# Optimization experiments

Measured on AMD Instinct MI355X. Metric: run time of the kernel, lower is better.

## Reference

```python
import jax, jax.numpy as jnp
import numpy as np

N, E = 20000, 320000
NFEAT, NHID = 512, 1024
DROPOUT_P = 0.5


def setup_inputs() -> dict:
    key = jax.random.key(0)
    ks = jax.random.split(key, 9)
    x = jax.random.normal(ks[0], (N, NFEAT), dtype=jnp.float32)
    W1 = jax.random.normal(ks[1], (NFEAT, NHID), dtype=jnp.float32) / np.sqrt(NFEAT)
    b1 = jnp.zeros((NHID,), dtype=jnp.float32)
    W2 = jax.random.normal(ks[2], (NHID, NFEAT), dtype=jnp.float32) / np.sqrt(NHID)
    b2 = jnp.zeros((NFEAT,), dtype=jnp.float32)
    adj_vals = jax.random.uniform(ks[3], (E,), dtype=jnp.float32)
    u_drop = jax.random.uniform(ks[4], (N, NHID), dtype=jnp.float32)
    src = jax.random.randint(ks[5], (E,), 0, N, dtype=jnp.int64)
    dst = jax.random.randint(ks[6], (E,), 0, N, dtype=jnp.int64)
    return {"x": x, "W1": W1, "b1": b1, "W2": W2, "b2": b2,
            "adj_vals": adj_vals, "u_drop": u_drop, "src": src, "dst": dst}


def _graph_conv(h, W, b, adj_vals, src, dst, n_nodes):
    # GraphConvolution: adj @ (h @ W) + b, with adj in COO form (src, dst, vals)
    support = h @ W                                   # [N, d_out]
    msgs = adj_vals[:, None] * support[src]           # [E, d_out]
    agg = jax.ops.segment_sum(msgs, dst, num_segments=n_nodes)
    return agg + b


def reference(x, W1, b1, W2, b2, adj_vals, u_drop, src, dst):
    h = jax.nn.relu(_graph_conv(x, W1, b1, adj_vals, src, dst, N))
    # inverted dropout (training=True), deterministic via u_drop
    keep = (u_drop > DROPOUT_P).astype(h.dtype) / (1.0 - DROPOUT_P)
    h = h * keep
    out = _graph_conv(h, W2, b2, adj_vals, src, dst, N)
    return out
```

## Files before the change

kernel.cpp:

```cpp
#include <hip/hip_runtime.h>
#include <hip/hip_bf16.h>

typedef __attribute__((ext_vector_type(8))) short short8;
typedef __attribute__((ext_vector_type(4))) float f32x4;

#define N_NODES 20000
#define N_EDGES 320000
#define NFEAT 512
#define NHID 1024
#define MBTOT 1252
#define SCAN_NB 79

__device__ __forceinline__ float bf2f(unsigned short u) {
    union { unsigned int i; float f; } c; c.i = ((unsigned int)u) << 16; return c.f;
}
__device__ __forceinline__ unsigned short f2bf(float f) {
    union { float f; unsigned int i; } c; c.f = f;
    unsigned int x = c.i;
    return (unsigned short)((x + 0x7fffu + ((x >> 16) & 1u)) >> 16);
}


__global__ void hist_kernel(const int* __restrict__ dst, int* __restrict__ deg, int E) {
    int e = blockIdx.x * 256 + threadIdx.x;
    if (e < E) atomicAdd(&deg[dst[e]], 1);
}

__global__ __launch_bounds__(256) void scan_a(const int* __restrict__ deg,
                                              int* __restrict__ rp,
                                              int* __restrict__ part, int n) {
    __shared__ int sd[256];
    int t = threadIdx.x;
    int i = blockIdx.x * 256 + t;
    int v = (i < n) ? deg[i] : 0;
    int acc = v;
    sd[t] = acc;
    __syncthreads();
    for (int off = 1; off < 256; off <<= 1) {
        int u = (t >= off) ? sd[t - off] : 0;
        __syncthreads();
        acc += u;
        sd[t] = acc;
        __syncthreads();
    }
    if (i < n) rp[i] = acc - v;
    if (t == 255) part[blockIdx.x] = acc;
}

__global__ __launch_bounds__(256) void scan_b(int* __restrict__ part, int nb) {
    __shared__ int sd[256];
    int t = threadIdx.x;
    int v = (t < nb) ? part[t] : 0;
    int acc = v;
    sd[t] = acc;
    __syncthreads();
    for (int off = 1; off < 256; off <<= 1) {
        int u = (t >= off) ? sd[t - off] : 0;
        __syncthreads();
        acc += u;
        sd[t] = acc;
        __syncthreads();
    }
    if (t < nb) part[t] = acc - v;
    if (t == 255) part[nb] = acc;
}

__global__ __launch_bounds__(256) void scan_c(int* __restrict__ rp, int* __restrict__ cursor,
                                              const int* __restrict__ part, int n, int nb) {
    int i = blockIdx.x * 256 + threadIdx.x;
    if (i < n) {
        int v = rp[i] + part[blockIdx.x];
        rp[i] = v;
        cursor[i] = v;
    }
    if (i == 0) rp[n] = part[nb];
}

__global__ void fill_kernel(const int* __restrict__ src, const int* __restrict__ dst,
                            const float* __restrict__ vals, int* __restrict__ cursor,
                            int2* __restrict__ csr_ov, int E) {
    int e = blockIdx.x * 256 + threadIdx.x;
    if (e < E) {
        int d = dst[e];
        int pos = atomicAdd(&cursor[d], 1);
        csr_ov[pos] = make_int2(src[e] << 10, __float_as_int(vals[e]));
    }
}


__device__ __forceinline__ void transpose_body(const float* __restrict__ W,
                                               unsigned short* __restrict__ Bp,
                                               int K, int N, int bid) {
    __shared__ float tile[32][33];
    const int KT = K >> 5;
    int ntx = N >> 5;
    int k0 = (bid / ntx) << 5;
    int n0 = (bid % ntx) << 5;
    int tx = threadIdx.x & 31, ty = threadIdx.x >> 5;
#pragma unroll
    for (int i = 0; i < 32; i += 8)
        tile[ty + i][tx] = W[(size_t)(k0 + ty + i) * N + n0 + tx];
    __syncthreads();
#pragma unroll
    for (int i = 0; i < 32; i += 8) {
        int n = n0 + ty + i;
        int k = k0 + tx;
        int nb = n >> 4, rl = n & 15;
        int kb = k >> 5, kq = (k & 31) >> 3, j = k & 7;
        Bp[((((size_t)nb * KT + kb) * 64) + kq * 16 + rl) * 8 + j] = f2bf(tile[tx][ty + i]);
    }
}

__global__ __launch_bounds__(256) void transpose2_kernel(const float* __restrict__ W1,
                                                         unsigned short* __restrict__ w1p,
                                                         const float* __restrict__ W2,
                                                         unsigned short* __restrict__ w2p) {
    if (blockIdx.x < 512) transpose_body(W1, w1p, NFEAT, NHID, blockIdx.x);
    else                  transpose_body(W2, w2p, NHID, NFEAT, blockIdx.x - 512);
}


__global__ __launch_bounds__(256) void prep_kernel(const float* __restrict__ x,
                                                   unsigned short* __restrict__ xb,
                                                   const float* __restrict__ u,
                                                   unsigned int* __restrict__ mask) {
    __shared__ unsigned char nib[256];
    int b = blockIdx.x;
    int t = threadIdx.x;
    if (b < 5000) {
        int i = b * 256 + t;
        f32x4 v0 = ((const f32x4*)x)[i * 2];
        f32x4 v1 = ((const f32x4*)x)[i * 2 + 1];
        short8 o;
#pragma unroll
        for (int j = 0; j < 4; ++j) {
            o[j]     = (short)f2bf(v0[j]);
            o[4 + j] = (short)f2bf(v1[j]);
        }
        ((short8*)xb)[i] = o;
    } else {
        size_t base = (size_t)(b - 5000) * 2048;
        f32x4 v0 = ((const f32x4*)(u + base))[t * 2];
        f32x4 v1 = ((const f32x4*)(u + base))[t * 2 + 1];
        unsigned n = 0;
#pragma unroll
        for (int j = 0; j < 4; ++j) {
            n |= (v0[j] > 0.5f ? 1u : 0u) << j;
            n |= (v1[j] > 0.5f ? 1u : 0u) << (4 + j);
        }
        nib[t] = (unsigned char)n;
        __syncthreads();
        if (t < 64) {
            unsigned w = (unsigned)nib[t * 4] | ((unsigned)nib[t * 4 + 1] << 8) |
                         ((unsigned)nib[t * 4 + 2] << 16) | ((unsigned)nib[t * 4 + 3] << 24);
            mask[base / 32 + t] = w;
        }
    }
}


__global__ __launch_bounds__(256) void agg1_kernel(const unsigned short* __restrict__ xbf,
                                                   const int2* __restrict__ csr_ov,
                                                   const int* __restrict__ row_ptr,
                                                   unsigned short* __restrict__ A1p) {
    const int c = blockIdx.x & 7;
    const int dbase = (blockIdx.x >> 3) * 32;
    const int wid = threadIdx.x >> 6;
    const int lane = threadIdx.x & 63;
    const int g = lane >> 3;
    const int s = lane & 7;
    const int d = dbase + wid * 8 + g;
    const int e0 = row_ptr[d], e1 = row_ptr[d + 1];
    const char* xc = (const char*)xbf + (c * 64 + s * 8) * 2;
    const int glane = g * 8;

    f32x4 a0 = {0.f, 0.f, 0.f, 0.f}, a1 = {0.f, 0.f, 0.f, 0.f};

    int offX = 0; float valX = 0.f;
    if (e0 + s < e1) { int2 t = csr_ov[e0 + s]; offX = t.x; valX = __int_as_float(t.y); }

    for (int eb = e0; eb < e1; eb += 8) {
        int offY = 0; float valY = 0.f;
        if (eb + 8 + s < e1) { int2 t = csr_ov[eb + 8 + s]; offY = t.x; valY = __int_as_float(t.y); }
        int cnt = e1 - eb; if (cnt > 8) cnt = 8;
        if (cnt == 8) {
            short8 w[8];
#pragma unroll
            for (int i = 0; i < 8; ++i)
                w[i] = *(const short8*)(xc + __shfl(offX, glane + i));
#pragma unroll
            for (int i = 0; i < 8; ++i) {
                float val = __shfl(valX, glane + i);
#pragma unroll
                for (int j = 0; j < 4; ++j) {
                    a0[j] += val * bf2f((unsigned short)w[i][j]);
                    a1[j] += val * bf2f((unsigned short)w[i][4 + j]);
                }
            }
        } else {
            for (int i = 0; i < cnt; ++i) {
                int off = __shfl(offX, glane + i);
                float val = __shfl(valX, glane + i);
                short8 w = *(const short8*)(xc + off);
#pragma unroll
                for (int j = 0; j < 4; ++j) {
                    a0[j] += val * bf2f((unsigned short)w[j]);
                    a1[j] += val * bf2f((unsigned short)w[4 + j]);
                }
            }
        }
        offX = offY; valX = valY;
    }
    short8 o;
#pragma unroll
    for (int j = 0; j < 4; ++j) {
        o[j]     = (short)f2bf(a0[j]);
        o[4 + j] = (short)f2bf(a1[j]);
    }
    size_t idx = ((((size_t)(d >> 4) * (NFEAT / 32) + (c * 2 + (s >> 2))) * 64) +
                  (s & 3) * 16 + (d & 15)) * 8;
    *(short8*)&A1p[idx] = o;
}


__global__ __launch_bounds__(256) void agg2_kernel(const unsigned short* __restrict__ s2,
                                                   const int2* __restrict__ csr_ov,
                                                   const int* __restrict__ row_ptr,
                                                   const float* __restrict__ b2,
                                                   float* __restrict__ out) {
    const int c = blockIdx.x & 7;
    const int dbase = (blockIdx.x >> 3) * 32;
    const int wid = threadIdx.x >> 6;
    const int lane = threadIdx.x & 63;
    const int g = lane >> 3;
    const int s = lane & 7;
    const int d = dbase + wid * 8 + g;
    const int e0 = row_ptr[d], e1 = row_ptr[d + 1];
    const int fb = c * 64 + s * 8;
    const char* xc = (const char*)s2 + fb * 2;
    const int glane = g * 8;

    f32x4 a0 = *(const f32x4*)&b2[fb];
    f32x4 a1 = *(const f32x4*)&b2[fb + 4];

    int offX = 0; float valX = 0.f;
    if (e0 + s < e1) { int2 t = csr_ov[e0 + s]; offX = t.x; valX = __int_as_float(t.y); }

    for (int eb = e0; eb < e1; eb += 8) {
        int offY = 0; float valY = 0.f;
        if (eb + 8 + s < e1) { int2 t = csr_ov[eb + 8 + s]; offY = t.x; valY = __int_as_float(t.y); }
        int cnt = e1 - eb; if (cnt > 8) cnt = 8;
        if (cnt == 8) {
            short8 w[8];
#pragma unroll
            for (int i = 0; i < 8; ++i)
                w[i] = *(const short8*)(xc + __shfl(offX, glane + i));
#pragma unroll
            for (int i = 0; i < 8; ++i) {
                float val = __shfl(valX, glane + i);
#pragma unroll
                for (int j = 0; j < 4; ++j) {
                    a0[j] += val * bf2f((unsigned short)w[i][j]);
                    a1[j] += val * bf2f((unsigned short)w[i][4 + j]);
                }
            }
        } else {
            for (int i = 0; i < cnt; ++i) {
                int off = __shfl(offX, glane + i);
                float val = __shfl(valX, glane + i);
                short8 w = *(const short8*)(xc + off);
#pragma unroll
                for (int j = 0; j < 4; ++j) {
                    a0[j] += val * bf2f((unsigned short)w[j]);
                    a1[j] += val * bf2f((unsigned short)w[4 + j]);
                }
            }
        }
        offX = offY; valX = valY;
    }
    *(f32x4*)&out[(size_t)d * NFEAT + fb]     = a0;
    *(f32x4*)&out[(size_t)d * NFEAT + fb + 4] = a1;
}


template <int EPI, int KT, int NW>
__global__ __launch_bounds__(256, 4) void gemm_pk(
    const unsigned short* __restrict__ Ap,
    const unsigned short* __restrict__ Bp,
    unsigned short* __restrict__ C,
    int M,
    const float* __restrict__ bias,
    const unsigned int* __restrict__ umask) {
    constexpr int N = NW * 64;
    constexpr int MI_MAX = 625;

    const int nwg = gridDim.x;
    const int bid = blockIdx.x;
    const int q = nwg >> 3, r = nwg & 7;
    const int xcd = bid & 7, pos = bid >> 3;
    const int swz = (xcd < r ? xcd * (q + 1) : r * (q + 1) + (xcd - r) * q) + pos;

    const int wid = threadIdx.x >> 6;
    const int lane = threadIdx.x & 63;
    const int rl = lane & 15;
    const int kq = lane >> 4;

    constexpr int NT2 = NW / 2;
    const int bm = swz / NT2;
    const int bn = swz % NT2;
    int mi = bm * 2 + (wid >> 1); if (mi >= MI_MAX) mi = MI_MAX - 1;
    const int ni = bn * 2 + (wid & 1);

    const unsigned short* ab = Ap + (size_t)(mi * 2) * KT * 512 + lane * 8;
    const unsigned short* bb = Bp + (size_t)(ni * 4) * KT * 512 + lane * 8;

    f32x4 acc[2][4] = {};
    short8 aX[2], bX[4], aY[2], bY[4];

#pragma unroll
    for (int m = 0; m < 2; ++m) aX[m] = *(const short8*)(ab + (size_t)m * KT * 512);
#pragma unroll
    for (int n = 0; n < 4; ++n) bX[n] = *(const short8*)(bb + (size_t)n * KT * 512);

#pragma unroll 1
    for (int kb = 0; kb < KT; kb += 2) {
#pragma unroll
        for (int m = 0; m < 2; ++m)
            aY[m] = *(const short8*)(ab + ((size_t)m * KT + kb + 1) * 512);
#pragma unroll
        for (int n = 0; n < 4; ++n)
            bY[n] = *(const short8*)(bb + ((size_t)n * KT + kb + 1) * 512);
#pragma unroll
        for (int m = 0; m < 2; ++m)
#pragma unroll
            for (int n = 0; n < 4; ++n)
                acc[m][n] = __builtin_amdgcn_mfma_f32_16x16x32_bf16(aX[m], bX[n], acc[m][n], 0, 0, 0);
        if (kb + 2 < KT) {
#pragma unroll
            for (int m = 0; m < 2; ++m)
                aX[m] = *(const short8*)(ab + ((size_t)m * KT + kb + 2) * 512);
#pragma unroll
            for (int n = 0; n < 4; ++n)
                bX[n] = *(const short8*)(bb + ((size_t)n * KT + kb + 2) * 512);
        }
#pragma unroll
        for (int m = 0; m < 2; ++m)
#pragma unroll
            for (int n = 0; n < 4; ++n)
                acc[m][n] = __builtin_amdgcn_mfma_f32_16x16x32_bf16(aY[m], bY[n], acc[m][n], 0, 0, 0);
    }

    if constexpr (EPI == 1) {
        __shared__ unsigned short ltr[4][32][40];
        constexpr int KT2 = N / 32;
#pragma unroll
        for (int n2 = 0; n2 < 2; ++n2) {
#pragma unroll
            for (int m = 0; m < 2; ++m) {
#pragma unroll
                for (int nn = 0; nn < 2; ++nn) {
                    int n = n2 * 2 + nn;
                    float bv = bias[ni * 64 + n * 16 + rl];
#pragma unroll
                    for (int j = 0; j < 4; ++j) {
                        float v = acc[m][n][j] + bv;
                        v = v > 0.f ? v : 0.f;
                        ltr[wid][m * 16 + kq * 4 + j][nn * 16 + rl] = f2bf(v);
                    }
                }
            }
            __builtin_amdgcn_s_waitcnt(0);
#pragma unroll
            for (int m2 = 0; m2 < 2; ++m2) {
                int row = m2 * 16 + rl;
                int gr = mi * 32 + row;
                unsigned w = umask[(size_t)gr * (N >> 5) + (ni * 2 + n2)];
                short8 u = *(const short8*)&ltr[wid][row][kq * 8];
                short8 o;
#pragma unroll
                for (int j = 0; j < 4; ++j) {
                    o[j]     = ((w >> (kq * 8 + j)) & 1u)
                               ? (short)f2bf(bf2f((unsigned short)u[j]) * 2.0f) : (short)0;
                    o[4 + j] = ((w >> (kq * 8 + 4 + j)) & 1u)
                               ? (short)f2bf(bf2f((unsigned short)u[4 + j]) * 2.0f) : (short)0;
                }
                int mbg = mi * 2 + m2;
                size_t dst = (((size_t)mbg * KT2 + (ni * 2 + n2)) * 64 + lane) * 8;
                *(short8*)&C[dst] = o;
            }
            __builtin_amdgcn_s_waitcnt(0);
        }
    } else {
        const int crow = kq * 4;
#pragma unroll
        for (int m = 0; m < 2; ++m) {
#pragma unroll
            for (int n = 0; n < 4; ++n) {
                int gr0 = mi * 32 + m * 16 + crow;
                int gc = ni * 64 + n * 16 + rl;
#pragma unroll
                for (int j = 0; j < 4; ++j) {
                    int gr = gr0 + j;
                    if (gr < M)
                        C[(size_t)gr * N + gc] = f2bf(acc[m][n][j]);
                }
            }
        }
    }
}


extern "C" void kernel_launch(void* const* d_in, const int* in_sizes, int n_in,
                              void* d_out, int out_size, void* d_ws, size_t ws_size,
                              hipStream_t stream) {
    const float* x        = (const float*)d_in[0];
    const float* W1       = (const float*)d_in[1];
    const float* b1       = (const float*)d_in[2];
    const float* W2       = (const float*)d_in[3];
    const float* b2       = (const float*)d_in[4];
    const float* adj_vals = (const float*)d_in[5];
    const float* u_drop   = (const float*)d_in[6];
    const int*   src      = (const int*)d_in[7];
    const int*   dst      = (const int*)d_in[8];
    float* out = (float*)d_out;

    char* p = (char*)d_ws;
    auto take = [&](size_t bytes) {
        char* q = p;
        p += (bytes + 255) & ~(size_t)255;
        return q;
    };
    int* deg        = (int*)take((size_t)N_NODES * 4);
    int* row_ptr    = (int*)take((size_t)(N_NODES + 1) * 4);
    int* cursor     = (int*)take((size_t)N_NODES * 4);
    int* part       = (int*)take((size_t)(SCAN_NB + 1) * 4);
    int2* csr_ov    = (int2*)take((size_t)N_EDGES * 8);
    unsigned short* w1p   = (unsigned short*)take((size_t)NFEAT * NHID * 2);
    unsigned short* w2p   = (unsigned short*)take((size_t)NFEAT * NHID * 2);
    unsigned short* xbf   = (unsigned short*)take((size_t)N_NODES * NFEAT * 2);
    unsigned short* a1p   = (unsigned short*)take((size_t)MBTOT * (NFEAT / 32) * 1024);
    unsigned short* a2p   = (unsigned short*)take((size_t)MBTOT * (NHID / 32) * 1024);
    unsigned short* s2buf = (unsigned short*)take((size_t)N_NODES * NFEAT * 2);
    unsigned int* umask   = (unsigned int*)take((size_t)N_NODES * (NHID / 32) * 4);

    hipMemsetAsync(deg, 0, (size_t)N_NODES * 4, stream);
    hist_kernel<<<(N_EDGES + 255) / 256, 256, 0, stream>>>(dst, deg, N_EDGES);
    scan_a<<<SCAN_NB, 256, 0, stream>>>(deg, row_ptr, part, N_NODES);
    scan_b<<<1, 256, 0, stream>>>(part, SCAN_NB);
    scan_c<<<SCAN_NB, 256, 0, stream>>>(row_ptr, cursor, part, N_NODES, SCAN_NB);
    fill_kernel<<<(N_EDGES + 255) / 256, 256, 0, stream>>>(src, dst, adj_vals, cursor,
                                                           csr_ov, N_EDGES);
    transpose2_kernel<<<1024, 256, 0, stream>>>(W1, w1p, W2, w2p);
    prep_kernel<<<15000, 256, 0, stream>>>(x, xbf, u_drop, umask);

    agg1_kernel<<<8 * 625, 256, 0, stream>>>(xbf, csr_ov, row_ptr, a1p);

    gemm_pk<1, NFEAT / 32, NHID / 64><<<313 * (NHID / 128), 256, 0, stream>>>(
        a1p, w1p, a2p, N_NODES, b1, umask);
    gemm_pk<0, NHID / 32, NFEAT / 64><<<313 * (NFEAT / 128), 256, 0, stream>>>(
        a2p, w2p, s2buf, N_NODES, nullptr, nullptr);

    agg2_kernel<<<8 * 625, 256, 0, stream>>>(s2buf, csr_ov, row_ptr, b2, out);
}
```

Measured before the change: 232.0 us.

## Merge prep, transpose and histogram launches; fuse mask build into agg1; drop shuffle prefetch

Combines the bf16 conversion of x, the two weight transposes and the degree histogram into one launch, and runs the dropout mask construction in the same launch as the first aggregation. This cuts the number of kernel launches and lets independent work fill the GPU together. Both aggregation kernels also drop the per-lane edge prefetch and shuffle broadcast, so every lane now loads the eight CSR entries directly. Those loads are redundant across lanes but served from cache, and the software prefetch of the next batch is lost.

New measurement: 244.8 us. 5.5% more time.

```diff
diff --git a/kernel.cpp b/kernel.cpp
--- a/kernel.cpp
+++ b/kernel.cpp
@@ -20,11 +20,6 @@
     return (unsigned short)((x + 0x7fffu + ((x >> 16) & 1u)) >> 16);
 }
 
-
-__global__ void hist_kernel(const int* __restrict__ dst, int* __restrict__ deg, int E) {
-    int e = blockIdx.x * 256 + threadIdx.x;
-    if (e < E) atomicAdd(&deg[dst[e]], 1);
-}
 
 __global__ __launch_bounds__(256) void scan_a(const int* __restrict__ deg,
                                               int* __restrict__ rp,
@@ -111,20 +106,14 @@
     }
 }
 
-__global__ __launch_bounds__(256) void transpose2_kernel(const float* __restrict__ W1,
-                                                         unsigned short* __restrict__ w1p,
-                                                         const float* __restrict__ W2,
-                                                         unsigned short* __restrict__ w2p) {
-    if (blockIdx.x < 512) transpose_body(W1, w1p, NFEAT, NHID, blockIdx.x);
-    else                  transpose_body(W2, w2p, NHID, NFEAT, blockIdx.x - 512);
-}
-
-
-__global__ __launch_bounds__(256) void prep_kernel(const float* __restrict__ x,
-                                                   unsigned short* __restrict__ xb,
-                                                   const float* __restrict__ u,
-                                                   unsigned int* __restrict__ mask) {
-    __shared__ unsigned char nib[256];
+__global__ __launch_bounds__(256) void p1_kernel(const float* __restrict__ x,
+                                                 unsigned short* __restrict__ xb,
+                                                 const float* __restrict__ W1,
+                                                 unsigned short* __restrict__ w1p,
+                                                 const float* __restrict__ W2,
+                                                 unsigned short* __restrict__ w2p,
+                                                 const int* __restrict__ dst,
+                                                 int* __restrict__ deg) {
     int b = blockIdx.x;
     int t = threadIdx.x;
     if (b < 5000) {
@@ -138,59 +127,69 @@
             o[4 + j] = (short)f2bf(v1[j]);
         }
         ((short8*)xb)[i] = o;
+    } else if (b < 5512) {
+        transpose_body(W1, w1p, NFEAT, NHID, b - 5000);
+    } else if (b < 6024) {
+        transpose_body(W2, w2p, NHID, NFEAT, b - 5512);
     } else {
+        int e = (b - 6024) * 256 + t;
+        if (e < N_EDGES) atomicAdd(&deg[dst[e]], 1);
+    }
+}
+
+
+__global__ __launch_bounds__(256) void p3_kernel(const unsigned short* __restrict__ xbf,
+                                                 const int2* __restrict__ csr_ov,
+                                                 const int* __restrict__ row_ptr,
+                                                 unsigned short* __restrict__ A1p,
+                                                 const float* __restrict__ u,
+                                                 unsigned int* __restrict__ mask) {
+    __shared__ unsigned char nib[256];
+    int b = blockIdx.x;
+    int tt = threadIdx.x;
+    if (b >= 5000) {
         size_t base = (size_t)(b - 5000) * 2048;
-        f32x4 v0 = ((const f32x4*)(u + base))[t * 2];
-        f32x4 v1 = ((const f32x4*)(u + base))[t * 2 + 1];
+        f32x4 v0 = ((const f32x4*)(u + base))[tt * 2];
+        f32x4 v1 = ((const f32x4*)(u + base))[tt * 2 + 1];
         unsigned n = 0;
 #pragma unroll
         for (int j = 0; j < 4; ++j) {
             n |= (v0[j] > 0.5f ? 1u : 0u) << j;
             n |= (v1[j] > 0.5f ? 1u : 0u) << (4 + j);
         }
-        nib[t] = (unsigned char)n;
+        nib[tt] = (unsigned char)n;
         __syncthreads();
-        if (t < 64) {
-            unsigned w = (unsigned)nib[t * 4] | ((unsigned)nib[t * 4 + 1] << 8) |
-                         ((unsigned)nib[t * 4 + 2] << 16) | ((unsigned)nib[t * 4 + 3] << 24);
-            mask[base / 32 + t] = w;
-        }
-    }
-}
-
-
-__global__ __launch_bounds__(256) void agg1_kernel(const unsigned short* __restrict__ xbf,
-                                                   const int2* __restrict__ csr_ov,
-                                                   const int* __restrict__ row_ptr,
-                                                   unsigned short* __restrict__ A1p) {
-    const int c = blockIdx.x & 7;
-    const int dbase = (blockIdx.x >> 3) * 32;
-    const int wid = threadIdx.x >> 6;
-    const int lane = threadIdx.x & 63;
+        if (tt < 64) {
+            unsigned w = (unsigned)nib[tt * 4] | ((unsigned)nib[tt * 4 + 1] << 8) |
+                         ((unsigned)nib[tt * 4 + 2] << 16) | ((unsigned)nib[tt * 4 + 3] << 24);
+            mask[base / 32 + tt] = w;
+        }
+        return;
+    }
+    const int c = b & 7;
+    const int dbase = (b >> 3) * 32;
+    const int wid = tt >> 6;
+    const int lane = tt & 63;
     const int g = lane >> 3;
     const int s = lane & 7;
     const int d = dbase + wid * 8 + g;
     const int e0 = row_ptr[d], e1 = row_ptr[d + 1];
     const char* xc = (const char*)xbf + (c * 64 + s * 8) * 2;
-    const int glane = g * 8;
 
     f32x4 a0 = {0.f, 0.f, 0.f, 0.f}, a1 = {0.f, 0.f, 0.f, 0.f};
 
-    int offX = 0; float valX = 0.f;
-    if (e0 + s < e1) { int2 t = csr_ov[e0 + s]; offX = t.x; valX = __int_as_float(t.y); }
-
     for (int eb = e0; eb < e1; eb += 8) {
-        int offY = 0; float valY = 0.f;
-        if (eb + 8 + s < e1) { int2 t = csr_ov[eb + 8 + s]; offY = t.x; valY = __int_as_float(t.y); }
         int cnt = e1 - eb; if (cnt > 8) cnt = 8;
         if (cnt == 8) {
+            int2 t[8];
+#pragma unroll
+            for (int i = 0; i < 8; ++i) t[i] = csr_ov[eb + i];
             short8 w[8];
 #pragma unroll
-            for (int i = 0; i < 8; ++i)
-                w[i] = *(const short8*)(xc + __shfl(offX, glane + i));
+            for (int i = 0; i < 8; ++i) w[i] = *(const short8*)(xc + t[i].x);
 #pragma unroll
             for (int i = 0; i < 8; ++i) {
-                float val = __shfl(valX, glane + i);
+                float val = __int_as_float(t[i].y);
 #pragma unroll
                 for (int j = 0; j < 4; ++j) {
                     a0[j] += val * bf2f((unsigned short)w[i][j]);
@@ -199,9 +198,9 @@
             }
         } else {
             for (int i = 0; i < cnt; ++i) {
-                int off = __shfl(offX, glane + i);
-                float val = __shfl(valX, glane + i);
-                short8 w = *(const short8*)(xc + off);
+                int2 t = csr_ov[eb + i];
+                float val = __int_as_float(t.y);
+                short8 w = *(const short8*)(xc + t.x);
 #pragma unroll
                 for (int j = 0; j < 4; ++j) {
                     a0[j] += val * bf2f((unsigned short)w[j]);
@@ -209,7 +208,6 @@
                 }
             }
         }
-        offX = offY; valX = valY;
     }
     short8 o;
 #pragma unroll
@@ -238,26 +236,22 @@
     const int e0 = row_ptr[d], e1 = row_ptr[d + 1];
     const int fb = c * 64 + s * 8;
     const char* xc = (const char*)s2 + fb * 2;
-    const int glane = g * 8;
 
     f32x4 a0 = *(const f32x4*)&b2[fb];
     f32x4 a1 = *(const f32x4*)&b2[fb + 4];
 
-    int offX = 0; float valX = 0.f;
-    if (e0 + s < e1) { int2 t = csr_ov[e0 + s]; offX = t.x; valX = __int_as_float(t.y); }
-
     for (int eb = e0; eb < e1; eb += 8) {
-        int offY = 0; float valY = 0.f;
-        if (eb + 8 + s < e1) { int2 t = csr_ov[eb + 8 + s]; offY = t.x; valY = __int_as_float(t.y); }
         int cnt = e1 - eb; if (cnt > 8) cnt = 8;
         if (cnt == 8) {
+            int2 t[8];
+#pragma unroll
+            for (int i = 0; i < 8; ++i) t[i] = csr_ov[eb + i];
             short8 w[8];
 #pragma unroll
-            for (int i = 0; i < 8; ++i)
-                w[i] = *(const short8*)(xc + __shfl(offX, glane + i));
+            for (int i = 0; i < 8; ++i) w[i] = *(const short8*)(xc + t[i].x);
 #pragma unroll
             for (int i = 0; i < 8; ++i) {
-                float val = __shfl(valX, glane + i);
+                float val = __int_as_float(t[i].y);
 #pragma unroll
                 for (int j = 0; j < 4; ++j) {
                     a0[j] += val * bf2f((unsigned short)w[i][j]);
@@ -266,9 +260,9 @@
             }
         } else {
             for (int i = 0; i < cnt; ++i) {
-                int off = __shfl(offX, glane + i);
-                float val = __shfl(valX, glane + i);
-                short8 w = *(const short8*)(xc + off);
+                int2 t = csr_ov[eb + i];
+                float val = __int_as_float(t.y);
+                short8 w = *(const short8*)(xc + t.x);
 #pragma unroll
                 for (int j = 0; j < 4; ++j) {
                     a0[j] += val * bf2f((unsigned short)w[j]);
@@ -276,7 +270,6 @@
                 }
             }
         }
-        offX = offY; valX = valY;
     }
     *(f32x4*)&out[(size_t)d * NFEAT + fb]     = a0;
     *(f32x4*)&out[(size_t)d * NFEAT + fb + 4] = a1;
@@ -444,16 +437,13 @@
     unsigned int* umask   = (unsigned int*)take((size_t)N_NODES * (NHID / 32) * 4);
 
     hipMemsetAsync(deg, 0, (size_t)N_NODES * 4, stream);
-    hist_kernel<<<(N_EDGES + 255) / 256, 256, 0, stream>>>(dst, deg, N_EDGES);
+    p1_kernel<<<7274, 256, 0, stream>>>(x, xbf, W1, w1p, W2, w2p, dst, deg);
     scan_a<<<SCAN_NB, 256, 0, stream>>>(deg, row_ptr, part, N_NODES);
     scan_b<<<1, 256, 0, stream>>>(part, SCAN_NB);
     scan_c<<<SCAN_NB, 256, 0, stream>>>(row_ptr, cursor, part, N_NODES, SCAN_NB);
     fill_kernel<<<(N_EDGES + 255) / 256, 256, 0, stream>>>(src, dst, adj_vals, cursor,
                                                            csr_ov, N_EDGES);
-    transpose2_kernel<<<1024, 256, 0, stream>>>(W1, w1p, W2, w2p);
-    prep_kernel<<<15000, 256, 0, stream>>>(x, xbf, u_drop, umask);
-
-    agg1_kernel<<<8 * 625, 256, 0, stream>>>(xbf, csr_ov, row_ptr, a1p);
+    p3_kernel<<<15000, 256, 0, stream>>>(xbf, csr_ov, row_ptr, a1p, u_drop, umask);
 
     gemm_pk<1, NFEAT / 32, NHID / 64><<<313 * (NHID / 128), 256, 0, stream>>>(
         a1p, w1p, a2p, N_NODES, b1, umask);
```

## Sort nodes by degree for aggregation balance and fuse prep kernels

Applied to the files above, without the earlier changes.

Builds a degree-sorted node permutation (a histogram over degree bins, a scan, then a scatter) and has both aggregation kernels process destination rows in that order, so each wave's 8 row-groups have similar edge counts and less lane divergence. The edge histogram, weight transposes, x conversion and dropout mask packing are merged into one launch to cut launch count. The cost is three extra small kernels plus an indirect perm lookup. Permuted rows also scatter output writes, which may reduce locality.

After: 330.6 us. +42.5%, slower.

```diff
diff --git a/kernel.cpp b/kernel.cpp
--- a/kernel.cpp
+++ b/kernel.cpp
@@ -10,6 +10,7 @@
 #define NHID 1024
 #define MBTOT 1252
 #define SCAN_NB 79
+#define DBINS 512
 
 __device__ __forceinline__ float bf2f(unsigned short u) {
     union { unsigned int i; float f; } c; c.i = ((unsigned int)u) << 16; return c.f;
@@ -20,11 +21,6 @@
     return (unsigned short)((x + 0x7fffu + ((x >> 16) & 1u)) >> 16);
 }
 
-
-__global__ void hist_kernel(const int* __restrict__ dst, int* __restrict__ deg, int E) {
-    int e = blockIdx.x * 256 + threadIdx.x;
-    if (e < E) atomicAdd(&deg[dst[e]], 1);
-}
 
 __global__ __launch_bounds__(256) void scan_a(const int* __restrict__ deg,
                                               int* __restrict__ rp,
@@ -88,6 +84,45 @@
 }
 
 
+__global__ __launch_bounds__(256) void dhist_kernel(const int* __restrict__ deg,
+                                                    int* __restrict__ dbins, int n) {
+    int i = blockIdx.x * 256 + threadIdx.x;
+    if (i < n) {
+        int dv = deg[i]; if (dv > DBINS - 1) dv = DBINS - 1;
+        atomicAdd(&dbins[dv], 1);
+    }
+}
+
+__global__ __launch_bounds__(DBINS) void dscan_kernel(int* __restrict__ dbins,
+                                                      int* __restrict__ dcur) {
+    __shared__ int sd[DBINS];
+    int t = threadIdx.x;
+    int v = dbins[t];
+    int acc = v;
+    sd[t] = acc;
+    __syncthreads();
+    for (int off = 1; off < DBINS; off <<= 1) {
+        int u = (t >= off) ? sd[t - off] : 0;
+        __syncthreads();
+        acc += u;
+        sd[t] = acc;
+        __syncthreads();
+    }
+    dcur[t] = acc - v;
+}
+
+__global__ __launch_bounds__(256) void dscatter_kernel(const int* __restrict__ deg,
+                                                       int* __restrict__ dcur,
+                                                       int* __restrict__ perm, int n) {
+    int i = blockIdx.x * 256 + threadIdx.x;
+    if (i < n) {
+        int dv = deg[i]; if (dv > DBINS - 1) dv = DBINS - 1;
+        int pos = atomicAdd(&dcur[dv], 1);
+        perm[pos] = i;
+    }
+}
+
+
 __device__ __forceinline__ void transpose_body(const float* __restrict__ W,
                                                unsigned short* __restrict__ Bp,
                                                int K, int N, int bid) {
@@ -111,19 +146,16 @@
     }
 }
 
-__global__ __launch_bounds__(256) void transpose2_kernel(const float* __restrict__ W1,
-                                                         unsigned short* __restrict__ w1p,
-                                                         const float* __restrict__ W2,
-                                                         unsigned short* __restrict__ w2p) {
-    if (blockIdx.x < 512) transpose_body(W1, w1p, NFEAT, NHID, blockIdx.x);
-    else                  transpose_body(W2, w2p, NHID, NFEAT, blockIdx.x - 512);
-}
-
-
-__global__ __launch_bounds__(256) void prep_kernel(const float* __restrict__ x,
-                                                   unsigned short* __restrict__ xb,
-                                                   const float* __restrict__ u,
-                                                   unsigned int* __restrict__ mask) {
+__global__ __launch_bounds__(256) void p1_kernel(const float* __restrict__ x,
+                                                 unsigned short* __restrict__ xb,
+                                                 const float* __restrict__ W1,
+                                                 unsigned short* __restrict__ w1p,
+                                                 const float* __restrict__ W2,
+                                                 unsigned short* __restrict__ w2p,
+                                                 const int* __restrict__ dst,
+                                                 int* __restrict__ deg,
+                                                 const float* __restrict__ u,
+                                                 unsigned int* __restrict__ mask) {
     __shared__ unsigned char nib[256];
     int b = blockIdx.x;
     int t = threadIdx.x;
@@ -138,8 +170,15 @@
             o[4 + j] = (short)f2bf(v1[j]);
         }
         ((short8*)xb)[i] = o;
+    } else if (b < 5512) {
+        transpose_body(W1, w1p, NFEAT, NHID, b - 5000);
+    } else if (b < 6024) {
+        transpose_body(W2, w2p, NHID, NFEAT, b - 5512);
+    } else if (b < 7274) {
+        int e = (b - 6024) * 256 + t;
+        if (e < N_EDGES) atomicAdd(&deg[dst[e]], 1);
     } else {
-        size_t base = (size_t)(b - 5000) * 2048;
+        size_t base = (size_t)(b - 7274) * 2048;
         f32x4 v0 = ((const f32x4*)(u + base))[t * 2];
         f32x4 v1 = ((const f32x4*)(u + base))[t * 2 + 1];
         unsigned n = 0;
@@ -162,6 +201,7 @@
 __global__ __launch_bounds__(256) void agg1_kernel(const unsigned short* __restrict__ xbf,
                                                    const int2* __restrict__ csr_ov,
                                                    const int* __restrict__ row_ptr,
+                                                   const int* __restrict__ perm,
                                                    unsigned short* __restrict__ A1p) {
     const int c = blockIdx.x & 7;
     const int dbase = (blockIdx.x >> 3) * 32;
@@ -169,7 +209,7 @@
     const int lane = threadIdx.x & 63;
     const int g = lane >> 3;
     const int s = lane & 7;
-    const int d = dbase + wid * 8 + g;
+    const int d = perm[dbase + wid * 8 + g];
     const int e0 = row_ptr[d], e1 = row_ptr[d + 1];
     const char* xc = (const char*)xbf + (c * 64 + s * 8) * 2;
     const int glane = g * 8;
@@ -226,6 +266,7 @@
 __global__ __launch_bounds__(256) void agg2_kernel(const unsigned short* __restrict__ s2,
                                                    const int2* __restrict__ csr_ov,
                                                    const int* __restrict__ row_ptr,
+                                                   const int* __restrict__ perm,
                                                    const float* __restrict__ b2,
                                                    float* __restrict__ out) {
     const int c = blockIdx.x & 7;
@@ -234,7 +275,7 @@
     const int lane = threadIdx.x & 63;
     const int g = lane >> 3;
     const int s = lane & 7;
-    const int d = dbase + wid * 8 + g;
+    const int d = perm[dbase + wid * 8 + g];
     const int e0 = row_ptr[d], e1 = row_ptr[d + 1];
     const int fb = c * 64 + s * 8;
     const char* xc = (const char*)s2 + fb * 2;
@@ -434,6 +475,9 @@
     int* row_ptr    = (int*)take((size_t)(N_NODES + 1) * 4);
     int* cursor     = (int*)take((size_t)N_NODES * 4);
     int* part       = (int*)take((size_t)(SCAN_NB + 1) * 4);
+    int* dbins      = (int*)take((size_t)DBINS * 4);
+    int* dcur       = (int*)take((size_t)DBINS * 4);
+    int* perm       = (int*)take((size_t)N_NODES * 4);
     int2* csr_ov    = (int2*)take((size_t)N_EDGES * 8);
     unsigned short* w1p   = (unsigned short*)take((size_t)NFEAT * NHID * 2);
     unsigned short* w2p   = (unsigned short*)take((size_t)NFEAT * NHID * 2);
@@ -444,21 +488,24 @@
     unsigned int* umask   = (unsigned int*)take((size_t)N_NODES * (NHID / 32) * 4);
 
     hipMemsetAsync(deg, 0, (size_t)N_NODES * 4, stream);
-    hist_kernel<<<(N_EDGES + 255) / 256, 256, 0, stream>>>(dst, deg, N_EDGES);
+    hipMemsetAsync(dbins, 0, (size_t)DBINS * 4, stream);
+    p1_kernel<<<17274, 256, 0, stream>>>(x, xbf, W1, w1p, W2, w2p, dst, deg,
+                                         u_drop, umask);
     scan_a<<<SCAN_NB, 256, 0, stream>>>(deg, row_ptr, part, N_NODES);
     scan_b<<<1, 256, 0, stream>>>(part, SCAN_NB);
     scan_c<<<SCAN_NB, 256, 0, stream>>>(row_ptr, cursor, part, N_NODES, SCAN_NB);
     fill_kernel<<<(N_EDGES + 255) / 256, 256, 0, stream>>>(src, dst, adj_vals, cursor,
                                                            csr_ov, N_EDGES);
-    transpose2_kernel<<<1024, 256, 0, stream>>>(W1, w1p, W2, w2p);
-    prep_kernel<<<15000, 256, 0, stream>>>(x, xbf, u_drop, umask);
-
-    agg1_kernel<<<8 * 625, 256, 0, stream>>>(xbf, csr_ov, row_ptr, a1p);
+    dhist_kernel<<<SCAN_NB, 256, 0, stream>>>(deg, dbins, N_NODES);
+    dscan_kernel<<<1, DBINS, 0, stream>>>(dbins, dcur);
+    dscatter_kernel<<<SCAN_NB, 256, 0, stream>>>(deg, dcur, perm, N_NODES);
+
+    agg1_kernel<<<8 * 625, 256, 0, stream>>>(xbf, csr_ov, row_ptr, perm, a1p);
 
     gemm_pk<1, NFEAT / 32, NHID / 64><<<313 * (NHID / 128), 256, 0, stream>>>(
         a1p, w1p, a2p, N_NODES, b1, umask);
     gemm_pk<0, NHID / 32, NFEAT / 64><<<313 * (NFEAT / 128), 256, 0, stream>>>(
         a2p, w2p, s2buf, N_NODES, nullptr, nullptr);
 
-    agg2_kernel<<<8 * 625, 256, 0, stream>>>(s2buf, csr_ov, row_ptr, b2, out);
-}
+    agg2_kernel<<<8 * 625, 256, 0, stream>>>(s2buf, csr_ov, row_ptr, perm, b2, out);
+}
```
